# Kernel optimization log

Measured on AMD Instinct MI355X. Metric: run time of the kernel, lower is better.

Reference implementation:

```python
import jax, jax.numpy as jnp
import numpy as np

N_CLASSES = 256
PER_CLASS = 128
N_SUPPORT = 5
N_QUERY = PER_CLASS - N_SUPPORT  # 123
N_VIEW = 2
D = 384
N = N_CLASSES * PER_CLASS  # 32768


def setup_inputs() -> dict:
    key = jax.random.key(0)
    k1, k2 = jax.random.split(key, 2)
    reps = jax.random.normal(k1, (N, N_VIEW, D), dtype=jnp.float32)
    # block-sorted labels: class c occupies rows [c*PER_CLASS, (c+1)*PER_CLASS)
    labels = (jnp.arange(N, dtype=jnp.int32) // PER_CLASS).astype(jnp.int32)
    return {"reps": reps, "labels": labels}


def reference(reps, labels):
    # labels are block-sorted per class, so the original's
    # labels.eq(c).nonzero()[:n_support] / [n_support:] gathers are static reshapes.
    reps_r = reps.reshape(N_CLASSES, PER_CLASS, N_VIEW, D)
    # class-mean prototypes over the support set: [C, V, D]
    prototypes = reps_r[:, :N_SUPPORT].mean(axis=1)
    # query samples: [C*N_QUERY, V, D]
    queries = reps_r[:, N_SUPPORT:].reshape(N_CLASSES * N_QUERY, N_VIEW, D)

    x2 = jnp.sum(queries * queries, axis=-1)            # [n, V]
    y2 = jnp.sum(prototypes * prototypes, axis=-1)      # [m, V]
    xy = jnp.einsum('nvd,mvd->nmv', queries, prototypes)  # [n, m, V]
    dists = x2[:, None, :] + y2[None, :, :] - 2.0 * xy

    # log_softmax over the prototype (class) axis
    log_p_y = jax.nn.log_softmax(-dists, axis=1)
    log_p_y = log_p_y.reshape(N_CLASSES, N_QUERY, N_CLASSES, N_VIEW)

    # gather the true-class log-prob for each query / view
    cls = jnp.arange(N_CLASSES)
    correct = log_p_y[cls, :, cls, :]  # [C, N_QUERY, V]
    loss = -correct.mean()
    return loss
```

## Files before the change

kernel.cpp:

```cpp
#include <hip/hip_runtime.h>
#include <hip/hip_bf16.h>
#include <math.h>

#define NCLS 256
#define PER_CLASS 128
#define NSUP 5
#define NQRY 123
#define NVIEW 2
#define DD 384
#define NQ_TOT (NCLS * NQRY)
#define BM 128
#define BK 64
#define RSTR 72

typedef __attribute__((ext_vector_type(8))) short short8;
typedef __attribute__((ext_vector_type(4))) float floatx4;

union FragU { uint4 u; short8 s; };
union PkU { __hip_bfloat162 b2; unsigned int u; };

__device__ __forceinline__ unsigned int cvt2bf(float lo, float hi) {
    PkU p;
    p.b2 = __float22bfloat162_rn(make_float2(lo, hi));
    return p.u;
}

__global__ __launch_bounds__(384) void proto_kernel(const float* __restrict__ reps,
                                                    ushort* __restrict__ pbf,
                                                    float* __restrict__ y2) {
    __shared__ float wp[6];
    const int b = blockIdx.x;
    const int c = b & 255, v = b >> 8;
    const int d = threadIdx.x;
    const float* p = reps + ((size_t)(c * PER_CLASS) * NVIEW + v) * DD + d;
    float s = 0.f;
#pragma unroll
    for (int k = 0; k < NSUP; ++k) s += p[(size_t)k * NVIEW * DD];
    s *= 0.2f;
    __hip_bfloat16 h = __float2bfloat16(s);
    pbf[(size_t)b * DD + d] = *reinterpret_cast<ushort*>(&h);
    float q = s * s;
#pragma unroll
    for (int o = 1; o < 64; o <<= 1) q += __shfl_xor(q, o);
    if ((d & 63) == 0) wp[d >> 6] = q;
    __syncthreads();
    if (d == 0) y2[b] = wp[0] + wp[1] + wp[2] + wp[3] + wp[4] + wp[5];
}

__global__ __launch_bounds__(256, 2) void main_kernel(const float* __restrict__ reps,
                                                      const ushort* __restrict__ pbf,
                                                      const float* __restrict__ y2g,
                                                      float* __restrict__ out) {
    __shared__ ushort q_lds[BM * RSTR];
    __shared__ ushort p_lds[NCLS * RSTR];
    __shared__ float pmx[BM][2];
    __shared__ float pse[BM][2];
    __shared__ float wred[8];

    const int t = threadIdx.x;
    const int v = blockIdx.y;
    const int q0 = blockIdx.x * BM;
    const int wave = t >> 6;
    const int lane = t & 63;
    const int col = lane & 15;
    const int quad = lane >> 4;
    const int wm = wave >> 1;
    const int wn = wave & 1;

    const int sq = t >> 1;
    const int h = (t & 1) * 32;
    const int nq = q0 + sq;
    const float* qsrc = reps +
        (size_t)((nq / NQRY) * PER_CLASS + NSUP + (nq % NQRY)) * (NVIEW * DD) + v * DD + h;
    const ushort* psrc = pbf + (size_t)(v * NCLS + t) * DD;
    ushort* qdst = &q_lds[sq * RSTR + h];
    ushort* pdst = &p_lds[t * RSTR];

    floatx4 acc[4][8];
#pragma unroll
    for (int mt = 0; mt < 4; ++mt)
#pragma unroll
        for (int nt = 0; nt < 8; ++nt) acc[mt][nt] = (floatx4)0.f;

    for (int kt = 0; kt < DD / BK; ++kt) {
        float4 qf[8];
        uint4 pl[8];
#pragma unroll
        for (int i = 0; i < 8; ++i) qf[i] = *(const float4*)(qsrc + kt * BK + i * 4);
#pragma unroll
        for (int i = 0; i < 8; ++i) pl[i] = ((const uint4*)(psrc + kt * BK))[i];
        uint4 qw[4];
#pragma unroll
        for (int i = 0; i < 4; ++i) {
            qw[i].x = cvt2bf(qf[2 * i].x, qf[2 * i].y);
            qw[i].y = cvt2bf(qf[2 * i].z, qf[2 * i].w);
            qw[i].z = cvt2bf(qf[2 * i + 1].x, qf[2 * i + 1].y);
            qw[i].w = cvt2bf(qf[2 * i + 1].z, qf[2 * i + 1].w);
        }

        if (kt) __syncthreads();
#pragma unroll
        for (int i = 0; i < 4; ++i) *(uint4*)(qdst + h * 0 + i * 8) = qw[i];
#pragma unroll
        for (int i = 0; i < 8; ++i) *(uint4*)(pdst + i * 8) = pl[i];
        __syncthreads();

#pragma unroll
        for (int ks = 0; ks < 2; ++ks) {
            short8 af[4];
#pragma unroll
            for (int mt = 0; mt < 4; ++mt) {
                FragU f;
                f.u = *(const uint4*)&q_lds[(wm * 64 + mt * 16 + col) * RSTR + ks * 32 + quad * 8];
                af[mt] = f.s;
            }
#pragma unroll
            for (int nt = 0; nt < 8; ++nt) {
                FragU b;
                b.u = *(const uint4*)&p_lds[(wn * 128 + nt * 16 + col) * RSTR + ks * 32 + quad * 8];
#pragma unroll
                for (int mt = 0; mt < 4; ++mt)
                    acc[mt][nt] = __builtin_amdgcn_mfma_f32_16x16x32_bf16(af[mt], b.s, acc[mt][nt], 0, 0, 0);
            }
        }
    }

    float y2c[8];
#pragma unroll
    for (int nt = 0; nt < 8; ++nt) y2c[nt] = y2g[v * NCLS + wn * 128 + nt * 16 + col];

    float corr = 0.f;
#pragma unroll
    for (int mt = 0; mt < 4; ++mt) {
#pragma unroll
        for (int r = 0; r < 4; ++r) {
            const int qloc = wm * 64 + mt * 16 + quad * 4 + r;
            const int n = q0 + qloc;
            const int cn = n / NQRY;
            float s[8];
            float mx = -1e30f;
#pragma unroll
            for (int nt = 0; nt < 8; ++nt) {
                s[nt] = 2.f * acc[mt][nt][r] - y2c[nt];
                mx = fmaxf(mx, s[nt]);
                if (cn == wn * 128 + nt * 16 + col) corr += s[nt];
            }
#pragma unroll
            for (int o = 1; o < 16; o <<= 1) mx = fmaxf(mx, __shfl_xor(mx, o));
            float e = 0.f;
#pragma unroll
            for (int nt = 0; nt < 8; ++nt) e += __expf(s[nt] - mx);
#pragma unroll
            for (int o = 1; o < 16; o <<= 1) e += __shfl_xor(e, o);
            if (col == 0) { pmx[qloc][wn] = mx; pse[qloc][wn] = e; }
        }
    }
#pragma unroll
    for (int o = 1; o < 64; o <<= 1) corr += __shfl_xor(corr, o);
    if (lane == 0) wred[wave] = corr;
    __syncthreads();

    float lval = 0.f;
    if (t < BM) {
        float m0 = pmx[t][0], m1 = pmx[t][1];
        float M = fmaxf(m0, m1);
        float E = pse[t][0] * __expf(m0 - M) + pse[t][1] * __expf(m1 - M);
        lval = M + __logf(E);
    }
#pragma unroll
    for (int o = 1; o < 64; o <<= 1) lval += __shfl_xor(lval, o);
    if (lane == 0) wred[4 + wave] = lval;
    __syncthreads();

    if (t == 0) {
        float tot = (wred[4] + wred[5] + wred[6] + wred[7]) -
                    (wred[0] + wred[1] + wred[2] + wred[3]);
        atomicAdd(out, tot * (1.f / (float)(NQ_TOT * NVIEW)));
    }
}

extern "C" void kernel_launch(void* const* d_in, const int* in_sizes, int n_in,
                              void* d_out, int out_size, void* d_ws, size_t ws_size,
                              hipStream_t stream) {
    const float* reps = (const float*)d_in[0];
    float* ws = (float*)d_ws;
    ushort* pbf = (ushort*)ws;
    float* y2 = (float*)(pbf + NVIEW * NCLS * DD);
    float* out = (float*)d_out;

    hipMemsetAsync(out, 0, sizeof(float), stream);
    proto_kernel<<<dim3(NVIEW * NCLS), dim3(DD), 0, stream>>>(reps, pbf, y2);
    main_kernel<<<dim3(NQ_TOT / BM, NVIEW), dim3(256), 0, stream>>>(reps, pbf, y2, out);
}
```

Measured before the change: 198.6 us.

## Pre-pack swizzled prototype tiles and load them directly to LDS

The prototype kernel now writes bf16 prototypes in a per-K-tile packed layout with an XOR swizzle on 8-element chunks. The main kernel copies each prototype tile straight from global memory into LDS with global_load_lds, skipping the register round trip, and reads B fragments through the matching swizzle instead of using a padded stride. This is meant to cut VGPR pressure and VALU/LDS-store work in the K loop and to avoid bank conflicts without padding. The load is async and shares the existing barrier, which relies on correct waitcnt handling.

```diff
diff --git a/kernel.cpp b/kernel.cpp
--- a/kernel.cpp
+++ b/kernel.cpp
@@ -11,7 +11,9 @@
 #define NQ_TOT (NCLS * NQRY)
 #define BM 128
 #define BK 64
+#define NKT (DD / BK)
 #define RSTR 72
+#define PTILE (NCLS * BK)
 
 typedef __attribute__((ext_vector_type(8))) short short8;
 typedef __attribute__((ext_vector_type(4))) float floatx4;
@@ -25,8 +27,14 @@
     return p.u;
 }
 
+__device__ __forceinline__ void load16(const void* g, void* l) {
+    __builtin_amdgcn_global_load_lds(
+        (const __attribute__((address_space(1))) unsigned int*)g,
+        (__attribute__((address_space(3))) unsigned int*)l, 16, 0, 0);
+}
+
 __global__ __launch_bounds__(384) void proto_kernel(const float* __restrict__ reps,
-                                                    ushort* __restrict__ pbf,
+                                                    ushort* __restrict__ ppk,
                                                     float* __restrict__ y2) {
     __shared__ float wp[6];
     const int b = blockIdx.x;
@@ -37,8 +45,13 @@
 #pragma unroll
     for (int k = 0; k < NSUP; ++k) s += p[(size_t)k * NVIEW * DD];
     s *= 0.2f;
-    __hip_bfloat16 h = __float2bfloat16(s);
-    pbf[(size_t)b * DD + d] = *reinterpret_cast<ushort*>(&h);
+    __hip_bfloat16 hh = __float2bfloat16(s);
+    const int kt = d >> 6;
+    const int ch = (d >> 3) & 7;
+    const int w = d & 7;
+    const int slot = ch ^ (c & 7);
+    ppk[((size_t)(v * NKT + kt) * NCLS + c) * BK + slot * 8 + w] =
+        *reinterpret_cast<ushort*>(&hh);
     float q = s * s;
 #pragma unroll
     for (int o = 1; o < 64; o <<= 1) q += __shfl_xor(q, o);
@@ -48,11 +61,11 @@
 }
 
 __global__ __launch_bounds__(256, 2) void main_kernel(const float* __restrict__ reps,
-                                                      const ushort* __restrict__ pbf,
+                                                      const ushort* __restrict__ ppk,
                                                       const float* __restrict__ y2g,
                                                       float* __restrict__ out) {
     __shared__ ushort q_lds[BM * RSTR];
-    __shared__ ushort p_lds[NCLS * RSTR];
+    __shared__ ushort p_lds[PTILE];
     __shared__ float pmx[BM][2];
     __shared__ float pse[BM][2];
     __shared__ float wred[8];
@@ -72,9 +85,9 @@
     const int nq = q0 + sq;
     const float* qsrc = reps +
         (size_t)((nq / NQRY) * PER_CLASS + NSUP + (nq % NQRY)) * (NVIEW * DD) + v * DD + h;
-    const ushort* psrc = pbf + (size_t)(v * NCLS + t) * DD;
     ushort* qdst = &q_lds[sq * RSTR + h];
-    ushort* pdst = &p_lds[t * RSTR];
+    const ushort* psrc = ppk + (size_t)v * NKT * PTILE + (wave * 8) * 512 + lane * 8;
+    ushort* pdst0 = &p_lds[(wave * 8) * 512];
 
     floatx4 acc[4][8];
 #pragma unroll
@@ -82,13 +95,10 @@
 #pragma unroll
         for (int nt = 0; nt < 8; ++nt) acc[mt][nt] = (floatx4)0.f;
 
-    for (int kt = 0; kt < DD / BK; ++kt) {
+    for (int kt = 0; kt < NKT; ++kt) {
         float4 qf[8];
-        uint4 pl[8];
 #pragma unroll
         for (int i = 0; i < 8; ++i) qf[i] = *(const float4*)(qsrc + kt * BK + i * 4);
-#pragma unroll
-        for (int i = 0; i < 8; ++i) pl[i] = ((const uint4*)(psrc + kt * BK))[i];
         uint4 qw[4];
 #pragma unroll
         for (int i = 0; i < 4; ++i) {
@@ -100,9 +110,10 @@
 
         if (kt) __syncthreads();
 #pragma unroll
-        for (int i = 0; i < 4; ++i) *(uint4*)(qdst + h * 0 + i * 8) = qw[i];
-#pragma unroll
-        for (int i = 0; i < 8; ++i) *(uint4*)(pdst + i * 8) = pl[i];
+        for (int i = 0; i < 8; ++i)
+            load16(psrc + (size_t)kt * PTILE + i * 512, pdst0 + i * 512);
+#pragma unroll
+        for (int i = 0; i < 4; ++i) *(uint4*)(qdst + i * 8) = qw[i];
         __syncthreads();
 
 #pragma unroll
@@ -117,7 +128,8 @@
 #pragma unroll
             for (int nt = 0; nt < 8; ++nt) {
                 FragU b;
-                b.u = *(const uint4*)&p_lds[(wn * 128 + nt * 16 + col) * RSTR + ks * 32 + quad * 8];
+                b.u = *(const uint4*)&p_lds[(wn * 128 + nt * 16 + col) * BK +
+                                            ((4 * ks + quad) ^ (col & 7)) * 8];
 #pragma unroll
                 for (int mt = 0; mt < 4; ++mt)
                     acc[mt][nt] = __builtin_amdgcn_mfma_f32_16x16x32_bf16(af[mt], b.s, acc[mt][nt], 0, 0, 0);
@@ -184,11 +196,11 @@
                               hipStream_t stream) {
     const float* reps = (const float*)d_in[0];
     float* ws = (float*)d_ws;
-    ushort* pbf = (ushort*)ws;
-    float* y2 = (float*)(pbf + NVIEW * NCLS * DD);
+    ushort* ppk = (ushort*)ws;
+    float* y2 = (float*)(ppk + NVIEW * NKT * PTILE);
     float* out = (float*)d_out;
 
     hipMemsetAsync(out, 0, sizeof(float), stream);
-    proto_kernel<<<dim3(NVIEW * NCLS), dim3(DD), 0, stream>>>(reps, pbf, y2);
-    main_kernel<<<dim3(NQ_TOT / BM, NVIEW), dim3(256), 0, stream>>>(reps, pbf, y2, out);
-}
+    proto_kernel<<<dim3(NVIEW * NCLS), dim3(DD), 0, stream>>>(reps, ppk, y2);
+    main_kernel<<<dim3(NQ_TOT / BM, NVIEW), dim3(256), 0, stream>>>(reps, ppk, y2, out);
+}
```

Result: faster. 166.4 us (-16.2%).

## Double-buffer LDS tiles with register prefetch and halve K tile

Applied to the files above, without the earlier changes.

Replaces the single-buffered K loop with double-buffered LDS tiles of half the K width. The next tile's global loads are issued before the current tile's MFMAs, and one custom barrier per iteration replaces the previous two __syncthreads. The goal is to hide global-load latency behind MFMA work and cut barrier overhead. In exchange there are twice as many iterations, a full unroll that increases code size, and a hand-written barrier that waits only on lgkmcnt, which is sufficient here because staged data already passes through registers.

```diff
diff --git a/kernel.cpp b/kernel.cpp
--- a/kernel.cpp
+++ b/kernel.cpp
@@ -10,8 +10,9 @@
 #define DD 384
 #define NQ_TOT (NCLS * NQRY)
 #define BM 128
-#define BK 64
-#define RSTR 72
+#define BK 32
+#define NKT (DD / BK)
+#define QS 40
 
 typedef __attribute__((ext_vector_type(8))) short short8;
 typedef __attribute__((ext_vector_type(4))) float floatx4;
@@ -24,6 +25,8 @@
     p.b2 = __float22bfloat162_rn(make_float2(lo, hi));
     return p.u;
 }
+
+#define BARRIER() asm volatile("s_waitcnt lgkmcnt(0)\n\ts_barrier" ::: "memory")
 
 __global__ __launch_bounds__(384) void proto_kernel(const float* __restrict__ reps,
                                                     ushort* __restrict__ pbf,
@@ -51,8 +54,8 @@
                                                       const ushort* __restrict__ pbf,
                                                       const float* __restrict__ y2g,
                                                       float* __restrict__ out) {
-    __shared__ ushort q_lds[BM * RSTR];
-    __shared__ ushort p_lds[NCLS * RSTR];
+    __shared__ ushort q_lds[2][BM * QS];
+    __shared__ ushort p_lds[2][NCLS * QS];
     __shared__ float pmx[BM][2];
     __shared__ float pse[BM][2];
     __shared__ float wred[8];
@@ -68,13 +71,11 @@
     const int wn = wave & 1;
 
     const int sq = t >> 1;
-    const int h = (t & 1) * 32;
+    const int h16 = (t & 1) * 16;
     const int nq = q0 + sq;
     const float* qsrc = reps +
-        (size_t)((nq / NQRY) * PER_CLASS + NSUP + (nq % NQRY)) * (NVIEW * DD) + v * DD + h;
+        (size_t)((nq / NQRY) * PER_CLASS + NSUP + (nq % NQRY)) * (NVIEW * DD) + v * DD + h16;
     const ushort* psrc = pbf + (size_t)(v * NCLS + t) * DD;
-    ushort* qdst = &q_lds[sq * RSTR + h];
-    ushort* pdst = &p_lds[t * RSTR];
 
     floatx4 acc[4][8];
 #pragma unroll
@@ -82,46 +83,57 @@
 #pragma unroll
         for (int nt = 0; nt < 8; ++nt) acc[mt][nt] = (floatx4)0.f;
 
-    for (int kt = 0; kt < DD / BK; ++kt) {
-        float4 qf[8];
-        uint4 pl[8];
-#pragma unroll
-        for (int i = 0; i < 8; ++i) qf[i] = *(const float4*)(qsrc + kt * BK + i * 4);
-#pragma unroll
-        for (int i = 0; i < 8; ++i) pl[i] = ((const uint4*)(psrc + kt * BK))[i];
-        uint4 qw[4];
-#pragma unroll
-        for (int i = 0; i < 4; ++i) {
-            qw[i].x = cvt2bf(qf[2 * i].x, qf[2 * i].y);
-            qw[i].y = cvt2bf(qf[2 * i].z, qf[2 * i].w);
-            qw[i].z = cvt2bf(qf[2 * i + 1].x, qf[2 * i + 1].y);
-            qw[i].w = cvt2bf(qf[2 * i + 1].z, qf[2 * i + 1].w);
-        }
-
-        if (kt) __syncthreads();
-#pragma unroll
-        for (int i = 0; i < 4; ++i) *(uint4*)(qdst + h * 0 + i * 8) = qw[i];
-#pragma unroll
-        for (int i = 0; i < 8; ++i) *(uint4*)(pdst + i * 8) = pl[i];
-        __syncthreads();
-
-#pragma unroll
-        for (int ks = 0; ks < 2; ++ks) {
-            short8 af[4];
-#pragma unroll
-            for (int mt = 0; mt < 4; ++mt) {
-                FragU f;
-                f.u = *(const uint4*)&q_lds[(wm * 64 + mt * 16 + col) * RSTR + ks * 32 + quad * 8];
-                af[mt] = f.s;
-            }
-#pragma unroll
-            for (int nt = 0; nt < 8; ++nt) {
-                FragU b;
-                b.u = *(const uint4*)&p_lds[(wn * 128 + nt * 16 + col) * RSTR + ks * 32 + quad * 8];
-#pragma unroll
-                for (int mt = 0; mt < 4; ++mt)
-                    acc[mt][nt] = __builtin_amdgcn_mfma_f32_16x16x32_bf16(af[mt], b.s, acc[mt][nt], 0, 0, 0);
-            }
+    float4 qf[4];
+    uint4 pl[4];
+
+#define LOADT(kt)                                                                  \
+    do {                                                                           \
+        _Pragma("unroll") for (int i = 0; i < 4; ++i)                              \
+            qf[i] = *(const float4*)(qsrc + (kt) * BK + i * 4);                    \
+        _Pragma("unroll") for (int i = 0; i < 4; ++i)                              \
+            pl[i] = *((const uint4*)(psrc + (kt) * BK) + i);                       \
+    } while (0)
+
+#define STAGE(b)                                                                   \
+    do {                                                                           \
+        uint4 qw0, qw1;                                                            \
+        qw0.x = cvt2bf(qf[0].x, qf[0].y); qw0.y = cvt2bf(qf[0].z, qf[0].w);        \
+        qw0.z = cvt2bf(qf[1].x, qf[1].y); qw0.w = cvt2bf(qf[1].z, qf[1].w);        \
+        qw1.x = cvt2bf(qf[2].x, qf[2].y); qw1.y = cvt2bf(qf[2].z, qf[2].w);        \
+        qw1.z = cvt2bf(qf[3].x, qf[3].y); qw1.w = cvt2bf(qf[3].z, qf[3].w);        \
+        *(uint4*)&q_lds[b][sq * QS + h16] = qw0;                                   \
+        *(uint4*)&q_lds[b][sq * QS + h16 + 8] = qw1;                               \
+        _Pragma("unroll") for (int i = 0; i < 4; ++i)                              \
+            *(uint4*)&p_lds[b][t * QS + i * 8] = pl[i];                            \
+    } while (0)
+
+#define COMPUTE(b)                                                                 \
+    do {                                                                           \
+        short8 af[4];                                                              \
+        _Pragma("unroll") for (int mt = 0; mt < 4; ++mt) {                         \
+            FragU f;                                                               \
+            f.u = *(const uint4*)&q_lds[b][(wm * 64 + mt * 16 + col) * QS + quad * 8]; \
+            af[mt] = f.s;                                                          \
+        }                                                                          \
+        _Pragma("unroll") for (int nt = 0; nt < 8; ++nt) {                         \
+            FragU bb;                                                              \
+            bb.u = *(const uint4*)&p_lds[b][(wn * 128 + nt * 16 + col) * QS + quad * 8]; \
+            _Pragma("unroll") for (int mt = 0; mt < 4; ++mt)                       \
+                acc[mt][nt] = __builtin_amdgcn_mfma_f32_16x16x32_bf16(af[mt], bb.s, acc[mt][nt], 0, 0, 0); \
+        }                                                                          \
+    } while (0)
+
+    LOADT(0);
+    STAGE(0);
+    LOADT(1);
+    BARRIER();
+#pragma unroll
+    for (int kt = 0; kt < NKT; ++kt) {
+        COMPUTE(kt & 1);
+        if (kt < NKT - 1) {
+            STAGE((kt + 1) & 1);
+            if (kt < NKT - 2) LOADT(kt + 2);
+            BARRIER();
         }
     }
 
```

New measurement: 166.0 us. 16.4% less time.

## Drop LDS staging; load MFMA fragments directly from global per wave

Applied to the files above, without the earlier changes.

The main kernel no longer stages query and prototype tiles through shared memory with block barriers. Each wave now owns 32 query rows across all 256 classes, loads its bf16 A and B fragments straight from global memory, and does the full log-sum-exp in registers, removing the cross-wave pmx/pse merge. This removes LDS traffic and barriers, but every wave re-reads the whole prototype matrix from global/L2 and uses strided uncoalesced fragment loads. Accumulator registers per thread stay at 128 floats.

```diff
diff --git a/kernel.cpp b/kernel.cpp
--- a/kernel.cpp
+++ b/kernel.cpp
@@ -9,9 +9,7 @@
 #define NVIEW 2
 #define DD 384
 #define NQ_TOT (NCLS * NQRY)
-#define BM 128
-#define BK 64
-#define RSTR 72
+#define NKT 12
 
 typedef __attribute__((ext_vector_type(8))) short short8;
 typedef __attribute__((ext_vector_type(4))) float floatx4;
@@ -51,132 +49,87 @@
                                                       const ushort* __restrict__ pbf,
                                                       const float* __restrict__ y2g,
                                                       float* __restrict__ out) {
-    __shared__ ushort q_lds[BM * RSTR];
-    __shared__ ushort p_lds[NCLS * RSTR];
-    __shared__ float pmx[BM][2];
-    __shared__ float pse[BM][2];
-    __shared__ float wred[8];
+    __shared__ float wred[4];
 
     const int t = threadIdx.x;
     const int v = blockIdx.y;
-    const int q0 = blockIdx.x * BM;
     const int wave = t >> 6;
     const int lane = t & 63;
     const int col = lane & 15;
     const int quad = lane >> 4;
-    const int wm = wave >> 1;
-    const int wn = wave & 1;
+    const int q0w = blockIdx.x * 128 + wave * 32;
 
-    const int sq = t >> 1;
-    const int h = (t & 1) * 32;
-    const int nq = q0 + sq;
-    const float* qsrc = reps +
-        (size_t)((nq / NQRY) * PER_CLASS + NSUP + (nq % NQRY)) * (NVIEW * DD) + v * DD + h;
-    const ushort* psrc = pbf + (size_t)(v * NCLS + t) * DD;
-    ushort* qdst = &q_lds[sq * RSTR + h];
-    ushort* pdst = &p_lds[t * RSTR];
+    const int r0 = q0w + col;
+    const int r1 = q0w + 16 + col;
+    const float* a0 = reps +
+        (size_t)((r0 / NQRY) * PER_CLASS + NSUP + (r0 % NQRY)) * (NVIEW * DD) + v * DD + quad * 8;
+    const float* a1 = reps +
+        (size_t)((r1 / NQRY) * PER_CLASS + NSUP + (r1 % NQRY)) * (NVIEW * DD) + v * DD + quad * 8;
+    const ushort* bb = pbf + (size_t)(v * NCLS + col) * DD + quad * 8;
 
-    floatx4 acc[4][8];
+    floatx4 acc[2][16];
 #pragma unroll
-    for (int mt = 0; mt < 4; ++mt)
+    for (int m = 0; m < 2; ++m)
 #pragma unroll
-        for (int nt = 0; nt < 8; ++nt) acc[mt][nt] = (floatx4)0.f;
-
-    for (int kt = 0; kt < DD / BK; ++kt) {
-        float4 qf[8];
-        uint4 pl[8];
-#pragma unroll
-        for (int i = 0; i < 8; ++i) qf[i] = *(const float4*)(qsrc + kt * BK + i * 4);
-#pragma unroll
-        for (int i = 0; i < 8; ++i) pl[i] = ((const uint4*)(psrc + kt * BK))[i];
-        uint4 qw[4];
-#pragma unroll
-        for (int i = 0; i < 4; ++i) {
-            qw[i].x = cvt2bf(qf[2 * i].x, qf[2 * i].y);
-            qw[i].y = cvt2bf(qf[2 * i].z, qf[2 * i].w);
-            qw[i].z = cvt2bf(qf[2 * i + 1].x, qf[2 * i + 1].y);
-            qw[i].w = cvt2bf(qf[2 * i + 1].z, qf[2 * i + 1].w);
-        }
-
-        if (kt) __syncthreads();
-#pragma unroll
-        for (int i = 0; i < 4; ++i) *(uint4*)(qdst + h * 0 + i * 8) = qw[i];
-#pragma unroll
-        for (int i = 0; i < 8; ++i) *(uint4*)(pdst + i * 8) = pl[i];
-        __syncthreads();
+        for (int nt = 0; nt < 16; ++nt) acc[m][nt] = (floatx4)0.f;
 
 #pragma unroll
-        for (int ks = 0; ks < 2; ++ks) {
-            short8 af[4];
+    for (int kt = 0; kt < NKT; ++kt) {
+        float4 f0 = *(const float4*)(a0 + kt * 32);
+        float4 f1 = *(const float4*)(a0 + kt * 32 + 4);
+        float4 g0 = *(const float4*)(a1 + kt * 32);
+        float4 g1 = *(const float4*)(a1 + kt * 32 + 4);
+        FragU A0, A1;
+        A0.u.x = cvt2bf(f0.x, f0.y); A0.u.y = cvt2bf(f0.z, f0.w);
+        A0.u.z = cvt2bf(f1.x, f1.y); A0.u.w = cvt2bf(f1.z, f1.w);
+        A1.u.x = cvt2bf(g0.x, g0.y); A1.u.y = cvt2bf(g0.z, g0.w);
+        A1.u.z = cvt2bf(g1.x, g1.y); A1.u.w = cvt2bf(g1.z, g1.w);
 #pragma unroll
-            for (int mt = 0; mt < 4; ++mt) {
-                FragU f;
-                f.u = *(const uint4*)&q_lds[(wm * 64 + mt * 16 + col) * RSTR + ks * 32 + quad * 8];
-                af[mt] = f.s;
-            }
-#pragma unroll
-            for (int nt = 0; nt < 8; ++nt) {
-                FragU b;
-                b.u = *(const uint4*)&p_lds[(wn * 128 + nt * 16 + col) * RSTR + ks * 32 + quad * 8];
-#pragma unroll
-                for (int mt = 0; mt < 4; ++mt)
-                    acc[mt][nt] = __builtin_amdgcn_mfma_f32_16x16x32_bf16(af[mt], b.s, acc[mt][nt], 0, 0, 0);
-            }
+        for (int nt = 0; nt < 16; ++nt) {
+            FragU B;
+            B.u = *(const uint4*)(bb + (size_t)nt * 16 * DD + kt * 32);
+            acc[0][nt] = __builtin_amdgcn_mfma_f32_16x16x32_bf16(A0.s, B.s, acc[0][nt], 0, 0, 0);
+            acc[1][nt] = __builtin_amdgcn_mfma_f32_16x16x32_bf16(A1.s, B.s, acc[1][nt], 0, 0, 0);
         }
     }
 
-    float y2c[8];
+    float y2c[16];
 #pragma unroll
-    for (int nt = 0; nt < 8; ++nt) y2c[nt] = y2g[v * NCLS + wn * 128 + nt * 16 + col];
+    for (int nt = 0; nt < 16; ++nt) y2c[nt] = y2g[v * NCLS + nt * 16 + col];
 
-    float corr = 0.f;
+    float corr = 0.f, lsum = 0.f;
 #pragma unroll
-    for (int mt = 0; mt < 4; ++mt) {
+    for (int m = 0; m < 2; ++m) {
 #pragma unroll
         for (int r = 0; r < 4; ++r) {
-            const int qloc = wm * 64 + mt * 16 + quad * 4 + r;
-            const int n = q0 + qloc;
-            const int cn = n / NQRY;
-            float s[8];
+            const int qn = q0w + m * 16 + quad * 4 + r;
+            const int cn = qn / NQRY;
+            float s[16];
             float mx = -1e30f;
 #pragma unroll
-            for (int nt = 0; nt < 8; ++nt) {
-                s[nt] = 2.f * acc[mt][nt][r] - y2c[nt];
+            for (int nt = 0; nt < 16; ++nt) {
+                s[nt] = 2.f * acc[m][nt][r] - y2c[nt];
                 mx = fmaxf(mx, s[nt]);
-                if (cn == wn * 128 + nt * 16 + col) corr += s[nt];
+                if (cn == nt * 16 + col) corr += s[nt];
             }
 #pragma unroll
             for (int o = 1; o < 16; o <<= 1) mx = fmaxf(mx, __shfl_xor(mx, o));
             float e = 0.f;
 #pragma unroll
-            for (int nt = 0; nt < 8; ++nt) e += __expf(s[nt] - mx);
+            for (int nt = 0; nt < 16; ++nt) e += __expf(s[nt] - mx);
 #pragma unroll
             for (int o = 1; o < 16; o <<= 1) e += __shfl_xor(e, o);
-            if (col == 0) { pmx[qloc][wn] = mx; pse[qloc][wn] = e; }
+            if (col == 0) lsum += mx + __logf(e);
         }
     }
+    float val = lsum - corr;
 #pragma unroll
-    for (int o = 1; o < 64; o <<= 1) corr += __shfl_xor(corr, o);
-    if (lane == 0) wred[wave] = corr;
+    for (int o = 1; o < 64; o <<= 1) val += __shfl_xor(val, o);
+    if (lane == 0) wred[wave] = val;
     __syncthreads();
-
-    float lval = 0.f;
-    if (t < BM) {
-        float m0 = pmx[t][0], m1 = pmx[t][1];
-        float M = fmaxf(m0, m1);
-        float E = pse[t][0] * __expf(m0 - M) + pse[t][1] * __expf(m1 - M);
-        lval = M + __logf(E);
-    }
-#pragma unroll
-    for (int o = 1; o < 64; o <<= 1) lval += __shfl_xor(lval, o);
-    if (lane == 0) wred[4 + wave] = lval;
-    __syncthreads();
-
-    if (t == 0) {
-        float tot = (wred[4] + wred[5] + wred[6] + wred[7]) -
-                    (wred[0] + wred[1] + wred[2] + wred[3]);
-        atomicAdd(out, tot * (1.f / (float)(NQ_TOT * NVIEW)));
-    }
+    if (t == 0)
+        atomicAdd(out, (wred[0] + wred[1] + wred[2] + wred[3]) *
+                           (1.f / (float)(NQ_TOT * NVIEW)));
 }
 
 extern "C" void kernel_launch(void* const* d_in, const int* in_sizes, int n_in,
@@ -190,5 +143,5 @@
 
     hipMemsetAsync(out, 0, sizeof(float), stream);
     proto_kernel<<<dim3(NVIEW * NCLS), dim3(DD), 0, stream>>>(reps, pbf, y2);
-    main_kernel<<<dim3(NQ_TOT / BM, NVIEW), dim3(256), 0, stream>>>(reps, pbf, y2, out);
+    main_kernel<<<dim3(NQ_TOT / 128, NVIEW), dim3(256), 0, stream>>>(reps, pbf, y2, out);
 }
```

Result: slower. 203.1 us (+2.2%).
